# Kernel tuning notes

Measured on AMD Instinct MI355X. Metric: run time of the kernel, lower is better.

## Reference

```python
import jax, jax.numpy as jnp
import numpy as np

EPS = 1e-6
NUM_HEADS = 16


def _layer_norm(x):
    # LayerNorm32: fp32 layernorm, eps=1e-6, no affine params
    m = jnp.mean(x, axis=-1, keepdims=True)
    v = jnp.var(x, axis=-1, keepdims=True)
    return (x - m) * jax.lax.rsqrt(v + EPS)


def setup_inputs() -> dict:
    key = jax.random.key(0)
    ks = jax.random.split(key, 6)
    B, L, C = 4, 2048, 1024
    H = 4 * C
    s = 0.02
    return {
        "x": jax.random.normal(ks[0], (B, L, C), dtype=jnp.float32),
        "qkv_w": jax.random.normal(ks[1], (C, 3 * C), dtype=jnp.float32) * s,
        "qkv_b": jnp.zeros((3 * C,), dtype=jnp.float32),
        "proj_w": jax.random.normal(ks[2], (C, C), dtype=jnp.float32) * s,
        "proj_b": jnp.zeros((C,), dtype=jnp.float32),
        "fc1_w": jax.random.normal(ks[3], (C, H), dtype=jnp.float32) * s,
        "fc1_b": jnp.zeros((H,), dtype=jnp.float32),
        "fc2_w": jax.random.normal(ks[4], (H, C), dtype=jnp.float32) * s,
        "fc2_b": jnp.zeros((C,), dtype=jnp.float32),
    }


def _block(x, qkv_w, qkv_b, proj_w, proj_b, fc1_w, fc1_b, fc2_w, fc2_b):
    B, L, C = x.shape
    Hn = NUM_HEADS
    D = C // Hn

    # --- attention branch (pre-norm) ---
    h = _layer_norm(x)
    qkv = h @ qkv_w + qkv_b                      # [B, L, 3C]
    qkv = qkv.reshape(B, L, 3, Hn, D)
    q, k, v = qkv[:, :, 0], qkv[:, :, 1], qkv[:, :, 2]  # [B, L, Hn, D]
    scale = 1.0 / jnp.sqrt(jnp.asarray(D, dtype=x.dtype))
    logits = jnp.einsum("bqhd,bkhd->bhqk", q, k) * scale
    attn = jax.nn.softmax(logits, axis=-1)
    o = jnp.einsum("bhqk,bkhd->bqhd", attn, v).reshape(B, L, C)
    o = o @ proj_w + proj_b
    x = x + o

    # --- MLP branch (pre-norm) ---
    h = _layer_norm(x)
    h = jax.nn.gelu(h @ fc1_w + fc1_b, approximate=True)  # tanh GELU
    h = h @ fc2_w + fc2_b
    return x + h


def reference(x, qkv_w, qkv_b, proj_w, proj_b, fc1_w, fc1_b, fc2_w, fc2_b):
    return _block(x, qkv_w, qkv_b, proj_w, proj_b, fc1_w, fc1_b, fc2_w, fc2_b)
```

## Files before the change

### kernel.cpp

```cpp
#include <hip/hip_runtime.h>
#include <hip/hip_bf16.h>

typedef float f32x4 __attribute__((ext_vector_type(4)));
typedef __bf16 bf16x8 __attribute__((ext_vector_type(8)));
typedef unsigned short us8 __attribute__((ext_vector_type(8)));

#define MBYTE (1ull << 20)

#define QSCALE_LOG2E 0.18033688011112042f

__device__ __forceinline__ unsigned short f2bf(float f) {
    __bf16 h = (__bf16)f;
    return __builtin_bit_cast(unsigned short, h);
}

__device__ __forceinline__ float fast_exp2(float x) {
    return __builtin_amdgcn_exp2f(x);
}

__device__ __forceinline__ f32x4 mfma16(bf16x8 a, bf16x8 b, f32x4 c) {
    return __builtin_amdgcn_mfma_f32_16x16x32_bf16(a, b, c, 0, 0, 0);
}

__device__ __forceinline__ void gload16(const void* g, void* l) {
    __builtin_amdgcn_global_load_lds(
        (const __attribute__((address_space(1))) unsigned int*)g,
        (__attribute__((address_space(3))) unsigned int*)l, 16, 0, 0);
}

__global__ __launch_bounds__(256) void ln_kernel(const float* __restrict__ x,
                                                 unsigned short* __restrict__ out) {
    int row = blockIdx.x;
    int t = threadIdx.x;
    const float* xr = x + (size_t)row * 1024;
    float4 v = *(const float4*)(xr + t * 4);
    float s = v.x + v.y + v.z + v.w;
    float ss = v.x * v.x + v.y * v.y + v.z * v.z + v.w * v.w;
    #pragma unroll
    for (int off = 1; off < 64; off <<= 1) {
        s += __shfl_xor(s, off);
        ss += __shfl_xor(ss, off);
    }
    __shared__ float ps[4], pss[4];
    int wid = t >> 6, lane = t & 63;
    if (lane == 0) { ps[wid] = s; pss[wid] = ss; }
    __syncthreads();
    s = ps[0] + ps[1] + ps[2] + ps[3];
    ss = pss[0] + pss[1] + pss[2] + pss[3];
    float mean = s * (1.0f / 1024.0f);
    float var = ss * (1.0f / 1024.0f) - mean * mean;
    float rs = rsqrtf(var + 1e-6f);
    ushort4 ov;
    ov.x = f2bf((v.x - mean) * rs);
    ov.y = f2bf((v.y - mean) * rs);
    ov.z = f2bf((v.z - mean) * rs);
    ov.w = f2bf((v.w - mean) * rs);
    *(ushort4*)(out + (size_t)row * 1024 + t * 4) = ov;
}

__global__ __launch_bounds__(256) void convT_kernel(const float* __restrict__ W,
                                                    unsigned short* __restrict__ Wt,
                                                    int K, int N) {
    __shared__ float tile[32][33];
    int t = threadIdx.x;
    int tx = t & 31, ty = t >> 5;
    int bx = blockIdx.x, by = blockIdx.y;
    #pragma unroll
    for (int r = 0; r < 4; r++) {
        int row = by * 32 + ty + r * 8;
        int col = bx * 32 + tx;
        tile[ty + r * 8][tx] = W[(size_t)row * N + col];
    }
    __syncthreads();
    #pragma unroll
    for (int r = 0; r < 4; r++) {
        int orow = bx * 32 + ty + r * 8;
        int ocol = by * 32 + tx;
        Wt[(size_t)orow * K + ocol] = f2bf(tile[tx][ty + r * 8]);
    }
}

__global__ __launch_bounds__(256) void vT_kernel(const unsigned short* __restrict__ qkv,
                                                 unsigned short* __restrict__ vT) {
    __shared__ unsigned short tile[32][34];
    int t = threadIdx.x;
    int tx = t & 31, ty = t >> 5;
    int lt = blockIdx.x, dt = blockIdx.y, bh = blockIdx.z;
    int b = bh >> 4, h = bh & 15;
    const unsigned short* src = qkv + (size_t)(b * 2048 + lt * 32) * 3072 + 2048 + h * 64 + dt * 32;
    #pragma unroll
    for (int r = 0; r < 4; r++)
        tile[ty + r * 8][tx] = src[(size_t)(ty + r * 8) * 3072 + tx];
    __syncthreads();
    int perm = (lt & 1) * 32 + ((tx >> 2) & 3) * 8 + ((tx >> 4) & 1) * 4 + (tx & 3);
    unsigned short* dst = vT + ((size_t)bh * 64 + dt * 32) * 2048 + (size_t)(lt >> 1) * 64;
    #pragma unroll
    for (int r = 0; r < 4; r++)
        dst[(size_t)(ty + r * 8) * 2048 + perm] = tile[tx][ty + r * 8];
}

template <int EPI>
__global__ __launch_bounds__(256) void gemm_bt(const unsigned short* __restrict__ A,
                                               const unsigned short* __restrict__ Bt,
                                               const float* __restrict__ bias,
                                               const float* __restrict__ res,
                                               float* __restrict__ outF,
                                               unsigned short* __restrict__ outB,
                                               int M, int N, int K) {
    __shared__ __align__(16) unsigned short As[128 * 32];
    __shared__ __align__(16) unsigned short Bs[128 * 32];
    int t = threadIdx.x;
    int lane = t & 63, wid = t >> 6;

    int gx = gridDim.x;
    int nwg = gx * gridDim.y;
    int orig = blockIdx.y * gx + blockIdx.x;
    int cpx = nwg >> 3;
    int swz = (orig & 7) * cpx + (orig >> 3);
    int bm = swz / gx, bn = swz % gx;

    int wm = wid >> 1, wn = wid & 1;
    f32x4 acc[4][4] = {};

    int sub = lane >> 2;
    int chunk = lane & 3;
    const unsigned short* gA0 = A + (size_t)(bm * 128 + wid * 32 + sub) * K + chunk * 8;
    const unsigned short* gA1 = gA0 + (size_t)16 * K;
    const unsigned short* gB0 = Bt + (size_t)(bn * 128 + wid * 32 + sub) * K + chunk * 8;
    const unsigned short* gB1 = gB0 + (size_t)16 * K;
    unsigned short* lA0 = &As[(wid * 32) * 32];
    unsigned short* lA1 = &As[(wid * 32 + 16) * 32];
    unsigned short* lB0 = &Bs[(wid * 32) * 32];
    unsigned short* lB1 = &Bs[(wid * 32 + 16) * 32];

    for (int k0 = 0; k0 < K; k0 += 32) {
        __syncthreads();
        gload16(gA0 + k0, lA0);
        gload16(gA1 + k0, lA1);
        gload16(gB0 + k0, lB0);
        gload16(gB1 + k0, lB1);
        __syncthreads();
        bf16x8 af[4], bfr[4];
        #pragma unroll
        for (int m = 0; m < 4; m++)
            af[m] = *(const bf16x8*)&As[(wm * 64 + m * 16 + (lane & 15)) * 32 + (lane >> 4) * 8];
        #pragma unroll
        for (int n = 0; n < 4; n++)
            bfr[n] = *(const bf16x8*)&Bs[(wn * 64 + n * 16 + (lane & 15)) * 32 + (lane >> 4) * 8];
        #pragma unroll
        for (int m = 0; m < 4; m++)
            #pragma unroll
            for (int n = 0; n < 4; n++)
                acc[m][n] = mfma16(af[m], bfr[n], acc[m][n]);
    }

    #pragma unroll
    for (int m = 0; m < 4; m++) {
        #pragma unroll
        for (int n = 0; n < 4; n++) {
            int col = bn * 128 + wn * 64 + n * 16 + (lane & 15);
            float bv = bias[col];
            #pragma unroll
            for (int r = 0; r < 4; r++) {
                int row = bm * 128 + wm * 64 + m * 16 + (lane >> 4) * 4 + r;
                float val = acc[m][n][r] + bv;
                if (EPI == 0) {
                    if (col < 1024) val *= QSCALE_LOG2E;
                    outB[(size_t)row * N + col] = f2bf(val);
                } else if (EPI == 1) {
                    float g = 0.5f * val *
                              (1.0f + tanhf(0.7978845608028654f *
                                            (val + 0.044715f * val * val * val)));
                    outB[(size_t)row * N + col] = f2bf(g);
                } else {
                    outF[(size_t)row * N + col] = val + res[(size_t)row * N + col];
                }
            }
        }
    }
}

__global__ __launch_bounds__(256) void attn_kernel(const unsigned short* __restrict__ qkv,
                                                   const unsigned short* __restrict__ vT,
                                                   unsigned short* __restrict__ o) {
    int bid = blockIdx.x;
    int qb = bid & 31;
    int bh = bid >> 5;
    int b = bh >> 4, h = bh & 15;
    int t = threadIdx.x, lane = t & 63, wid = t >> 6;

    const unsigned short* base = qkv + (size_t)b * 2048 * 3072 + h * 64;
    const unsigned short* vbase = vT + (size_t)bh * 64 * 2048;

    __shared__ __align__(16) unsigned short Ks[2][64][32];
    __shared__ __align__(16) unsigned short Vs[2][64][32];

    int ql = lane & 15;
    int hi = lane >> 4;

    bf16x8 qf[2];
    {
        int qrow = qb * 64 + wid * 16 + ql;
        const unsigned short* qp = base + (size_t)qrow * 3072 + hi * 8;
        qf[0] = *(const bf16x8*)(qp);
        qf[1] = *(const bf16x8*)(qp + 32);
    }

    float m_r = -1e30f, lpart = 0.0f;
    f32x4 accO[4] = {};

    int srow = wid * 16 + (lane >> 2);
    int schunk = (lane & 3) * 8;
    const unsigned short* gk = base + 1024 + (size_t)srow * 3072 + schunk;
    const unsigned short* gv = vbase + (size_t)srow * 2048 + schunk;
    unsigned short* lK0 = &Ks[0][wid * 16][0];
    unsigned short* lK1 = &Ks[1][wid * 16][0];
    unsigned short* lV0 = &Vs[0][wid * 16][0];
    unsigned short* lV1 = &Vs[1][wid * 16][0];

    for (int kt = 0; kt < 32; kt++) {
        __syncthreads();
        gload16(gk, lK0);
        gload16(gk + 32, lK1);
        gload16(gv, lV0);
        gload16(gv + 32, lV1);
        gk += (size_t)64 * 3072;
        gv += 64;
        __syncthreads();

        f32x4 s0 = {}, s1 = {}, s2 = {}, s3 = {};
        #pragma unroll
        for (int c = 0; c < 2; c++) {
            bf16x8 a0 = *(const bf16x8*)&Ks[c][ 0 + ql][hi * 8];
            bf16x8 a1 = *(const bf16x8*)&Ks[c][16 + ql][hi * 8];
            bf16x8 a2 = *(const bf16x8*)&Ks[c][32 + ql][hi * 8];
            bf16x8 a3 = *(const bf16x8*)&Ks[c][48 + ql][hi * 8];
            s0 = mfma16(a0, qf[c], s0);
            s1 = mfma16(a1, qf[c], s1);
            s2 = mfma16(a2, qf[c], s2);
            s3 = mfma16(a3, qf[c], s3);
        }

        float mx = fmaxf(fmaxf(fmaxf(s0[0], s0[1]), fmaxf(s0[2], s0[3])),
                         fmaxf(fmaxf(s1[0], s1[1]), fmaxf(s1[2], s1[3])));
        mx = fmaxf(mx, fmaxf(fmaxf(s2[0], s2[1]), fmaxf(s2[2], s2[3])));
        mx = fmaxf(mx, fmaxf(fmaxf(s3[0], s3[1]), fmaxf(s3[2], s3[3])));
        if (!__all(mx <= m_r + 8.0f)) {
            float mm = fmaxf(mx, __shfl_xor(mx, 16));
            mm = fmaxf(mm, __shfl_xor(mm, 32));
            float mnew = fmaxf(m_r, mm);
            float corr = fast_exp2(m_r - mnew);
            m_r = mnew;
            lpart *= corr;
            #pragma unroll
            for (int r = 0; r < 4; r++) {
                float cq = __shfl(corr, hi * 4 + r);
                accO[0][r] *= cq; accO[1][r] *= cq;
                accO[2][r] *= cq; accO[3][r] *= cq;
            }
        }

        us8 pu0, pu1;
        #pragma unroll
        for (int j = 0; j < 4; j++) {
            float pa = fast_exp2(s0[j] - m_r);
            float pb = fast_exp2(s1[j] - m_r);
            float pc = fast_exp2(s2[j] - m_r);
            float pd = fast_exp2(s3[j] - m_r);
            lpart += (pa + pb) + (pc + pd);
            pu0[j] = f2bf(pa); pu0[4 + j] = f2bf(pb);
            pu1[j] = f2bf(pc); pu1[4 + j] = f2bf(pd);
        }
        bf16x8 paf0 = __builtin_bit_cast(bf16x8, pu0);
        bf16x8 paf1 = __builtin_bit_cast(bf16x8, pu1);

        #pragma unroll
        for (int nn = 0; nn < 4; nn++) {
            bf16x8 bv0 = *(const bf16x8*)&Vs[0][nn * 16 + ql][hi * 8];
            bf16x8 bv1 = *(const bf16x8*)&Vs[1][nn * 16 + ql][hi * 8];
            accO[nn] = mfma16(paf0, bv0, accO[nn]);
            accO[nn] = mfma16(paf1, bv1, accO[nn]);
        }
    }

    lpart += __shfl_xor(lpart, 16);
    lpart += __shfl_xor(lpart, 32);
    float rinv = 1.0f / lpart;
    #pragma unroll
    for (int r = 0; r < 4; r++) {
        float rq = __shfl(rinv, hi * 4 + r);
        int row = qb * 64 + wid * 16 + hi * 4 + r;
        #pragma unroll
        for (int nn = 0; nn < 4; nn++) {
            int col = h * 64 + nn * 16 + ql;
            o[(size_t)(b * 2048 + row) * 1024 + col] = f2bf(accO[nn][r] * rq);
        }
    }
}

extern "C" void kernel_launch(void* const* d_in, const int* in_sizes, int n_in,
                              void* d_out, int out_size, void* d_ws, size_t ws_size,
                              hipStream_t stream) {
    const float* x      = (const float*)d_in[0];
    const float* qkv_w  = (const float*)d_in[1];
    const float* qkv_b  = (const float*)d_in[2];
    const float* proj_w = (const float*)d_in[3];
    const float* proj_b = (const float*)d_in[4];
    const float* fc1_w  = (const float*)d_in[5];
    const float* fc1_b  = (const float*)d_in[6];
    const float* fc2_w  = (const float*)d_in[7];
    const float* fc2_b  = (const float*)d_in[8];
    float* out = (float*)d_out;

    char* ws = (char*)d_ws;
    unsigned short* h_buf   = (unsigned short*)(ws + 0 * MBYTE);
    unsigned short* qkv_buf = (unsigned short*)(ws + 16 * MBYTE);
    unsigned short* o_buf   = (unsigned short*)(ws + 64 * MBYTE);
    float*          x2_buf  = (float*)(ws + 80 * MBYTE);
    unsigned short* vT_buf  = (unsigned short*)(ws + 80 * MBYTE);
    unsigned short* wqT     = (unsigned short*)(ws + 112 * MBYTE);
    unsigned short* wpT     = (unsigned short*)(ws + 118 * MBYTE);
    unsigned short* w1T     = (unsigned short*)(ws + 120 * MBYTE);
    unsigned short* w2T     = (unsigned short*)(ws + 128 * MBYTE);
    unsigned short* g_buf   = (unsigned short*)(ws + 16 * MBYTE);

    const int M = 8192;

    convT_kernel<<<dim3(3072 / 32, 1024 / 32), 256, 0, stream>>>(qkv_w, wqT, 1024, 3072);
    convT_kernel<<<dim3(1024 / 32, 1024 / 32), 256, 0, stream>>>(proj_w, wpT, 1024, 1024);
    convT_kernel<<<dim3(4096 / 32, 1024 / 32), 256, 0, stream>>>(fc1_w, w1T, 1024, 4096);
    convT_kernel<<<dim3(1024 / 32, 4096 / 32), 256, 0, stream>>>(fc2_w, w2T, 4096, 1024);

    ln_kernel<<<M, 256, 0, stream>>>(x, h_buf);

    gemm_bt<0><<<dim3(3072 / 128, M / 128), 256, 0, stream>>>(
        h_buf, wqT, qkv_b, nullptr, nullptr, qkv_buf, M, 3072, 1024);

    vT_kernel<<<dim3(64, 2, 64), 256, 0, stream>>>(qkv_buf, vT_buf);

    attn_kernel<<<dim3(32 * 64), 256, 0, stream>>>(qkv_buf, vT_buf, o_buf);

    gemm_bt<2><<<dim3(1024 / 128, M / 128), 256, 0, stream>>>(
        o_buf, wpT, proj_b, x, x2_buf, nullptr, M, 1024, 1024);

    ln_kernel<<<M, 256, 0, stream>>>(x2_buf, h_buf);

    gemm_bt<1><<<dim3(4096 / 128, M / 128), 256, 0, stream>>>(
        h_buf, w1T, fc1_b, nullptr, nullptr, g_buf, M, 4096, 1024);

    gemm_bt<2><<<dim3(1024 / 128, M / 128), 256, 0, stream>>>(
        g_buf, w2T, fc2_b, x2_buf, out, nullptr, M, 1024, 4096);
}
```

Before: 472.4 us.

## Double-buffer GEMM LDS tiles, XOR-swizzle LDS layout, and use exp2-based GELU

Converts the bf16 GEMM main loop to a two-stage LDS double buffer, so global-to-LDS loads for the next K tile are issued before the MFMAs on the current tile, with one barrier per iteration instead of two. The LDS chunk layout is XOR-swizzled on both the write and read side to reduce bank conflicts on fragment loads. MFMA issue is wrapped in s_setprio. The tanh GELU epilogue is rewritten as x*sigmoid(2k*w) using a hardware exp2, which is mathematically equivalent to the tanh form but cheaper. LDS use per block doubles, which can reduce occupancy.

```diff
diff --git a/kernel.cpp b/kernel.cpp
--- a/kernel.cpp
+++ b/kernel.cpp
@@ -8,6 +8,7 @@
 #define MBYTE (1ull << 20)
 
 #define QSCALE_LOG2E 0.18033688011112042f
+#define GELU_K 2.3022081902f
 
 __device__ __forceinline__ unsigned short f2bf(float f) {
     __bf16 h = (__bf16)f;
@@ -107,8 +108,8 @@
                                                float* __restrict__ outF,
                                                unsigned short* __restrict__ outB,
                                                int M, int N, int K) {
-    __shared__ __align__(16) unsigned short As[128 * 32];
-    __shared__ __align__(16) unsigned short Bs[128 * 32];
+    __shared__ __align__(16) unsigned short As[2][128 * 32];
+    __shared__ __align__(16) unsigned short Bs[2][128 * 32];
     int t = threadIdx.x;
     int lane = t & 63, wid = t >> 6;
 
@@ -123,42 +124,55 @@
     f32x4 acc[4][4] = {};
 
     int sub = lane >> 2;
-    int chunk = lane & 3;
-    const unsigned short* gA0 = A + (size_t)(bm * 128 + wid * 32 + sub) * K + chunk * 8;
+    int schunk = ((lane & 3) ^ ((lane >> 3) & 3)) * 8;
+    const unsigned short* gA0 = A + (size_t)(bm * 128 + wid * 32 + sub) * K + schunk;
     const unsigned short* gA1 = gA0 + (size_t)16 * K;
-    const unsigned short* gB0 = Bt + (size_t)(bn * 128 + wid * 32 + sub) * K + chunk * 8;
+    const unsigned short* gB0 = Bt + (size_t)(bn * 128 + wid * 32 + sub) * K + schunk;
     const unsigned short* gB1 = gB0 + (size_t)16 * K;
-    unsigned short* lA0 = &As[(wid * 32) * 32];
-    unsigned short* lA1 = &As[(wid * 32 + 16) * 32];
-    unsigned short* lB0 = &Bs[(wid * 32) * 32];
-    unsigned short* lB1 = &Bs[(wid * 32 + 16) * 32];
-
-    for (int k0 = 0; k0 < K; k0 += 32) {
-        __syncthreads();
-        gload16(gA0 + k0, lA0);
-        gload16(gA1 + k0, lA1);
-        gload16(gB0 + k0, lB0);
-        gload16(gB1 + k0, lB1);
-        __syncthreads();
+
+    int ql = lane & 15;
+    int rchunk = (((lane >> 4) ^ ((lane >> 1) & 3))) * 8;
+
+    const int NT = K >> 5;
+    gload16(gA0, &As[0][(wid * 32) * 32]);
+    gload16(gA1, &As[0][(wid * 32 + 16) * 32]);
+    gload16(gB0, &Bs[0][(wid * 32) * 32]);
+    gload16(gB1, &Bs[0][(wid * 32 + 16) * 32]);
+    __syncthreads();
+
+    int cur = 0;
+    for (int tt = 0; tt < NT; ++tt) {
+        if (tt + 1 < NT) {
+            int k0 = (tt + 1) << 5;
+            int nb = cur ^ 1;
+            gload16(gA0 + k0, &As[nb][(wid * 32) * 32]);
+            gload16(gA1 + k0, &As[nb][(wid * 32 + 16) * 32]);
+            gload16(gB0 + k0, &Bs[nb][(wid * 32) * 32]);
+            gload16(gB1 + k0, &Bs[nb][(wid * 32 + 16) * 32]);
+        }
         bf16x8 af[4], bfr[4];
         #pragma unroll
         for (int m = 0; m < 4; m++)
-            af[m] = *(const bf16x8*)&As[(wm * 64 + m * 16 + (lane & 15)) * 32 + (lane >> 4) * 8];
+            af[m] = *(const bf16x8*)&As[cur][(wm * 64 + m * 16 + ql) * 32 + rchunk];
         #pragma unroll
         for (int n = 0; n < 4; n++)
-            bfr[n] = *(const bf16x8*)&Bs[(wn * 64 + n * 16 + (lane & 15)) * 32 + (lane >> 4) * 8];
+            bfr[n] = *(const bf16x8*)&Bs[cur][(wn * 64 + n * 16 + ql) * 32 + rchunk];
+        __builtin_amdgcn_s_setprio(1);
         #pragma unroll
         for (int m = 0; m < 4; m++)
             #pragma unroll
             for (int n = 0; n < 4; n++)
                 acc[m][n] = mfma16(af[m], bfr[n], acc[m][n]);
+        __builtin_amdgcn_s_setprio(0);
+        __syncthreads();
+        cur ^= 1;
     }
 
     #pragma unroll
     for (int m = 0; m < 4; m++) {
         #pragma unroll
         for (int n = 0; n < 4; n++) {
-            int col = bn * 128 + wn * 64 + n * 16 + (lane & 15);
+            int col = bn * 128 + wn * 64 + n * 16 + ql;
             float bv = bias[col];
             #pragma unroll
             for (int r = 0; r < 4; r++) {
@@ -168,9 +182,8 @@
                     if (col < 1024) val *= QSCALE_LOG2E;
                     outB[(size_t)row * N + col] = f2bf(val);
                 } else if (EPI == 1) {
-                    float g = 0.5f * val *
-                              (1.0f + tanhf(0.7978845608028654f *
-                                            (val + 0.044715f * val * val * val)));
+                    float w = val + 0.044715f * val * val * val;
+                    float g = val / (1.0f + fast_exp2(-GELU_K * w));
                     outB[(size_t)row * N + col] = f2bf(g);
                 } else {
                     outF[(size_t)row * N + col] = val + res[(size_t)row * N + col];
```

Measured after the change: 449.0 us. 1.05x faster.
